# Performance work log

Hardware: AMD Instinct MI355X
Metric: run time of the kernel (lower is better)

The kernel has to match this reference:

```python
import jax, jax.numpy as jnp
import numpy as np

TOPK = 8
N_EXPERTS = 64
ALPHA = 0.001


def setup_inputs() -> dict:
    key = jax.random.key(0)
    k1, k2 = jax.random.split(key)
    B, S, H = 4, 4096, 4096
    x = jax.random.normal(k1, (B, S, H), dtype=jnp.float32)
    # kaiming-uniform-ish router weight, bound = sqrt(6/((1+5)*H)) = 1/sqrt(H)
    bound = 1.0 / np.sqrt(H)
    weight = jax.random.uniform(k2, (N_EXPERTS, H), dtype=jnp.float32,
                                minval=-bound, maxval=bound)
    return {"x": x, "weight": weight}


def reference(x, weight):
    B, S, H = x.shape
    E = weight.shape[0]
    tokens = x.reshape(-1, H)                      # (T, H), T = B*S
    logits = jnp.einsum('th,eh->te', tokens, weight)  # router GEMM (T, E)
    scores = jax.nn.softmax(logits, axis=-1)
    # top-k selection (torch uses sorted=False; same set of values/indices)
    topk_weight, topk_idx = jax.lax.top_k(scores, TOPK)  # (T, k)
    # normalize top-k probs (norm_topk_prob=True, topk>1)
    topk_weight = topk_weight / (topk_weight.sum(axis=1, keepdims=True) + 1e-20)
    # seq-aux load-balancing loss (training path, alpha > 0, seq_aux=True)
    idx_flat = topk_idx.reshape(B, S * TOPK)                 # (B, S*k)
    ce = jax.nn.one_hot(idx_flat, E, dtype=jnp.float32).sum(axis=1)  # scatter_add of ones
    ce = ce / (S * TOPK / E)                                  # (B, E)
    mean_scores = scores.reshape(B, S, E).mean(axis=1)        # (B, E)
    aux_loss = (ce * mean_scores).sum(axis=1).mean() * ALPHA
    return topk_idx, topk_weight, aux_loss
```

## Files before the change

kernel.cpp:

```cpp
#include <hip/hip_runtime.h>
#include <math.h>

#define H 4096
#define NE 64
#define KTOP 8
#define TTOT 16384
#define BT1 32
#define NB1 (TTOT / BT1)
#define BT2 64
#define NB2 (TTOT / BT2)
#define TAU 1e-4f
#define DELTA 1e-3f

typedef __attribute__((ext_vector_type(8))) short bf16x8;
typedef __attribute__((ext_vector_type(4))) float f32x4;

union U4S8 { uint4 u; bf16x8 s; };

__device__ __forceinline__ unsigned bf16_rne(float f) {
  unsigned b = __float_as_uint(f);
  b += 0x7fffu + ((b >> 16) & 1u);
  return b >> 16;
}

__global__ __launch_bounds__(256) void w_prep(const float* __restrict__ w,
                                              uint4* __restrict__ wsimg) {
  const int sid = blockIdx.x * 256 + threadIdx.x;
  const int e = sid >> 9;
  const int rem = sid & 511;
  const int c = rem >> 2;
  const int s = rem & 3;
  const float* src = w + (size_t)e * H + c * 32 + s * 8;
  float4 f0 = *(const float4*)src;
  float4 f1 = *(const float4*)(src + 4);
  float xf[8] = {f0.x, f0.y, f0.z, f0.w, f1.x, f1.y, f1.z, f1.w};
  unsigned hu[8], lu[8];
#pragma unroll
  for (int j = 0; j < 8; ++j) {
    hu[j] = bf16_rne(xf[j]);
    float hf = __uint_as_float(hu[j] << 16);
    lu[j] = bf16_rne(xf[j] - hf);
  }
  uint4 hp, lp;
  hp.x = hu[0] | (hu[1] << 16); hp.y = hu[2] | (hu[3] << 16);
  hp.z = hu[4] | (hu[5] << 16); hp.w = hu[6] | (hu[7] << 16);
  lp.x = lu[0] | (lu[1] << 16); lp.y = lu[2] | (lu[3] << 16);
  lp.z = lu[4] | (lu[5] << 16); lp.w = lu[6] | (lu[7] << 16);
  const int slotp = s ^ ((e >> 1) & 3);
  wsimg[(size_t)c * 256 + e * 4 + slotp] = hp;
  wsimg[(size_t)128 * 256 + (size_t)c * 256 + e * 4 + slotp] = lp;
}

__device__ __forceinline__ void cvt_split(const float4 a, const float4 b,
                                          bf16x8* hi, bf16x8* lo) {
  float xf[8] = {a.x, a.y, a.z, a.w, b.x, b.y, b.z, b.w};
  unsigned ph[4], pl[4];
#pragma unroll
  for (int q = 0; q < 4; ++q)
    asm("v_cvt_pk_bf16_f32 %0, %1, %2" : "=v"(ph[q])
        : "v"(xf[2 * q]), "v"(xf[2 * q + 1]));
  float rs[8];
#pragma unroll
  for (int q = 0; q < 4; ++q) {
    rs[2 * q]     = xf[2 * q]     - __uint_as_float(ph[q] << 16);
    rs[2 * q + 1] = xf[2 * q + 1] - __uint_as_float(ph[q] & 0xffff0000u);
  }
#pragma unroll
  for (int q = 0; q < 4; ++q)
    asm("v_cvt_pk_bf16_f32 %0, %1, %2" : "=v"(pl[q])
        : "v"(rs[2 * q]), "v"(rs[2 * q + 1]));
  U4S8 h, l;
  h.u = (uint4){ph[0], ph[1], ph[2], ph[3]};
  l.u = (uint4){pl[0], pl[1], pl[2], pl[3]};
  *hi = h.s;
  *lo = l.s;
}

#define GLDS(GP, LP)                                                   \
  __builtin_amdgcn_global_load_lds(                                    \
      (const __attribute__((address_space(1))) void*)(GP),             \
      (__attribute__((address_space(3))) void*)(LP), 16, 0, 0)

__global__ __launch_bounds__(128, 1) void moe_pass1(
    const float* __restrict__ x, const uint4* __restrict__ wsimg,
    float* __restrict__ out, unsigned* __restrict__ wmask,
    float* __restrict__ waux) {
  extern __shared__ __align__(16) char smraw[];
  const int tid = threadIdx.x;
  const int lane = tid & 63;
  const int wid = tid >> 6;
  const int tok0 = blockIdx.x * BT1;
  const int trow = lane & 15;
  const int kgrp = lane >> 4;

  const char* xsrc[4];
#pragma unroll
  for (int q = 0; q < 4; ++q) {
    const int a = q * 2048 + tid * 16;
    const int tile = a >> 12;
    const int row = (a >> 8) & 15;
    const int inrow = a & 255;
    const int sin = inrow ^ ((row & 7) << 4);
    xsrc[q] = (const char*)(x + (size_t)(tok0 + tile * 16 + row) * H) + sin;
  }
  const uint4* wsrc[8];
  int wdst[8];
#pragma unroll
  for (int j = 0; j < 8; ++j) {
    const int hilo = j >> 2, sub = (j >> 1) & 1, half = j & 1;
    wsrc[j] = wsimg + (size_t)hilo * (128 * 256) + sub * 256 + half * 128 + tid;
    wdst[j] = 8192 + hilo * 8192 + sub * 4096 + half * 2048 + tid * 16;
  }

  f32x4 acc[4];
#pragma unroll
  for (int et = 0; et < 4; ++et) acc[et] = (f32x4){0.f, 0.f, 0.f, 0.f};

#define ISSUE_STEP(KC, BUF)                                              \
  do {                                                                   \
    char* bb = smraw + (size_t)(BUF) * 24576;                            \
    _Pragma("unroll") for (int q = 0; q < 4; ++q)                        \
      GLDS(xsrc[q] + (size_t)(KC) * 256, bb + q * 2048 + tid * 16);      \
    _Pragma("unroll") for (int j = 0; j < 8; ++j)                        \
      GLDS((const char*)(wsrc[j] + (size_t)(KC) * 512), bb + wdst[j]);   \
  } while (0)

  ISSUE_STEP(0, 0);
  ISSUE_STEP(1, 1);

  const int sx = (trow & 7) << 4;
  const int abase = wid * 4096 + trow * 256;
  int entry[4];
#pragma unroll
  for (int et = 0; et < 4; ++et) {
    const int e = et * 16 + trow;
    entry[et] = (e * 4 + (kgrp ^ ((e >> 1) & 3))) * 16;
  }

#pragma unroll 1
  for (int kc = 0; kc < 64; ++kc) {
    if (kc < 63) {
      asm volatile("s_waitcnt vmcnt(12)" ::: "memory");
    } else {
      asm volatile("s_waitcnt vmcnt(0)" ::: "memory");
    }
    __builtin_amdgcn_s_barrier();
    asm volatile("" ::: "memory");
    if (kc + 2 < 64) ISSUE_STEP(kc + 2, (kc + 2) % 3);

    const char* bufp = smraw + (size_t)(kc % 3) * 24576;
#pragma unroll
    for (int sub = 0; sub < 2; ++sub) {
      float4 v0 = *(const float4*)(bufp + abase + ((sub * 128 + kgrp * 32) ^ sx));
      float4 v1 = *(const float4*)(bufp + abase + ((sub * 128 + kgrp * 32 + 16) ^ sx));
      bf16x8 ah, al;
      cvt_split(v0, v1, &ah, &al);
#pragma unroll
      for (int et = 0; et < 4; ++et) {
        U4S8 bh, bl;
        bh.u = *(const uint4*)(bufp + 8192 + sub * 4096 + entry[et]);
        bl.u = *(const uint4*)(bufp + 16384 + sub * 4096 + entry[et]);
        acc[et] = __builtin_amdgcn_mfma_f32_16x16x32_bf16(ah, bh.s, acc[et], 0, 0, 0);
        acc[et] = __builtin_amdgcn_mfma_f32_16x16x32_bf16(ah, bl.s, acc[et], 0, 0, 0);
        acc[et] = __builtin_amdgcn_mfma_f32_16x16x32_bf16(al, bh.s, acc[et], 0, 0, 0);
      }
    }
  }

  __syncthreads();
  float* lg = (float*)smraw;
  float* msumA = (float*)(smraw + 8448);
  float* cntA = (float*)(smraw + 8960);
#pragma unroll
  for (int et = 0; et < 4; ++et)
#pragma unroll
    for (int r = 0; r < 4; ++r)
      lg[(wid * 16 + kgrp * 4 + r) * 66 + et * 16 + trow] = acc[et][r];
  __syncthreads();

  float msum = 0.f;
  int cnt = 0;
#pragma unroll 1
  for (int it = 0; it < 16; ++it) {
    const int t = wid * 16 + it;
    const float lf = lg[t * 66 + lane];

    float m = lf;
#pragma unroll
    for (int off = 32; off; off >>= 1) m = fmaxf(m, __shfl_xor(m, off));
    float p = expf(lf - m);
    float s = p;
#pragma unroll
    for (int off = 32; off; off >>= 1) s += __shfl_xor(s, off);
    msum += p / s;

    float cur = lf;
    float myv = 0.f;
    int myi = 0;
#pragma unroll
    for (int r = 0; r < 9; ++r) {
      float v = cur;
      int ix = lane;
#pragma unroll
      for (int off = 1; off < 64; off <<= 1) {
        float ov = __shfl_xor(v, off);
        int oi = __shfl_xor(ix, off);
        if (ov > v || (ov == v && oi < ix)) { v = ov; ix = oi; }
      }
      if (lane == r) { myv = v; myi = ix; }
      if (r < 8 && lane == ix) { cur = -INFINITY; ++cnt; }
    }

    const float m0 = __shfl(myv, 0);
    float e = expf(myv - m0);
    float sv = e;
    sv += __shfl_xor(sv, 1);
    sv += __shfl_xor(sv, 2);
    sv += __shfl_xor(sv, 4);
    const float wgtv = e / sv;
    const int tg = tok0 + t;
    if (lane < KTOP) {
      out[(size_t)tg * KTOP + lane] = (float)myi;
      out[(size_t)TTOT * KTOP + (size_t)tg * KTOP + lane] = wgtv;
    }

    const float nxt = __shfl(myv, (lane + 1) & 63);
    const bool gp = (lane < 8) && (myv - nxt < TAU);
    const unsigned long long anyg = __ballot(gp);
    const float v7 = __shfl(myv, 7);
    const unsigned long long msk = __ballot(lf >= v7 - DELTA);
    if (lane == 0) {
      const unsigned long long mv = anyg ? msk : 0ULL;
      wmask[tg] = (unsigned)mv;
      wmask[TTOT + tg] = (unsigned)(mv >> 32);
    }
  }
  msumA[wid * 64 + lane] = msum;
  cntA[wid * 64 + lane] = (float)cnt;
  __syncthreads();
  if (tid < 64) {
    waux[blockIdx.x * 128 + tid] = cntA[tid] + cntA[64 + tid];
    waux[blockIdx.x * 128 + 64 + tid] = msumA[tid] + msumA[64 + tid];
  }
}

__global__ __launch_bounds__(256) void moe_pass2(
    const float* __restrict__ x, const float* __restrict__ w,
    const unsigned* __restrict__ wmask, float* __restrict__ out) {
  __shared__ unsigned slo[64], shi[64];
  __shared__ double red[4];
  __shared__ double cval[64];
  __shared__ int cidx[64];
  const int tid = threadIdx.x;
  const int lane = tid & 63, wid = tid >> 6;
  const int t0 = blockIdx.x * BT2;

  if (tid < 64) { slo[tid] = wmask[t0 + tid]; shi[tid] = wmask[TTOT + t0 + tid]; }
  __syncthreads();
  int myf = (tid < 64) ? ((slo[tid] | shi[tid]) != 0u) : 0;
  if (!__syncthreads_or(myf)) return;

#pragma unroll 1
  for (int tt = 0; tt < BT2; ++tt) {
    const unsigned lo = slo[tt], hi = shi[tt];
    if (!(lo | hi)) continue;
    const int t = t0 + tt;
    const unsigned long long m = ((unsigned long long)hi << 32) | lo;
    const float* xr = x + (size_t)t * H;
    int ncand = 0;
#pragma unroll 1
    for (int e = 0; e < 64; ++e) {
      if (!((m >> e) & 1ULL)) continue;
      const float* wr = w + (size_t)e * H;
      double d = 0.0;
#pragma unroll
      for (int q = 0; q < 16; ++q) {
        const int k = tid + 256 * q;
        d = fma((double)xr[k], (double)wr[k], d);
      }
#pragma unroll
      for (int off = 32; off; off >>= 1) d += __shfl_xor(d, off);
      if (lane == 0) red[wid] = d;
      __syncthreads();
      if (tid == 0) {
        cval[ncand] = red[0] + red[1] + red[2] + red[3];
        cidx[ncand] = e;
      }
      __syncthreads();
      ++ncand;
    }
    if (tid == 0) {
      double sel[8];
      int si[8];
      for (int r = 0; r < 8; ++r) {
        int best = 0;
        double bv = -1e300;
        for (int c2 = 0; c2 < ncand; ++c2)
          if (cval[c2] > bv) { bv = cval[c2]; best = c2; }
        sel[r] = cval[best]; si[r] = cidx[best];
        cval[best] = -1e301;
      }
      const double m0 = sel[0];
      float es[8], ssum = 0.f;
      for (int r = 0; r < 8; ++r) { es[r] = expf((float)(sel[r] - m0)); ssum += es[r]; }
      for (int r = 0; r < 8; ++r) {
        out[(size_t)t * KTOP + r] = (float)si[r];
        out[(size_t)TTOT * KTOP + (size_t)t * KTOP + r] = es[r] / ssum;
      }
    }
    __syncthreads();
  }
}

__global__ __launch_bounds__(256) void moe_gate_aux(
    const float* __restrict__ waux, float* __restrict__ out) {
  const int tid = threadIdx.x;
  const int b = tid >> 6, e = tid & 63;
  float cnt = 0.f, ms = 0.f;
#pragma unroll 4
  for (int j = 0; j < 128; ++j) {
    const int blk = b * 128 + j;
    cnt += waux[blk * 128 + e];
    ms += waux[blk * 128 + 64 + e];
  }
  float term = (cnt * (1.f / 512.f)) * (ms * (1.f / 4096.f));
  __shared__ float red[4];
#pragma unroll
  for (int off = 32; off; off >>= 1) term += __shfl_xor(term, off);
  if ((tid & 63) == 0) red[tid >> 6] = term;
  __syncthreads();
  if (tid == 0) {
    float tot = red[0] + red[1] + red[2] + red[3];
    out[(size_t)TTOT * KTOP * 2] = tot * (0.001f / 4.f);
  }
}

extern "C" void kernel_launch(void* const* d_in, const int* in_sizes, int n_in,
                              void* d_out, int out_size, void* d_ws, size_t ws_size,
                              hipStream_t stream) {
  (void)in_sizes; (void)n_in; (void)out_size; (void)ws_size;
  const float* x = (const float*)d_in[0];
  const float* w = (const float*)d_in[1];
  float* out = (float*)d_out;
  uint4* wsimg = (uint4*)d_ws;
  unsigned* wmask = (unsigned*)((char*)d_ws + (1 << 21));
  float* waux = (float*)((char*)d_ws + (1 << 21) + 2 * TTOT * 4);
  (void)hipFuncSetAttribute((const void*)moe_pass1,
                            hipFuncAttributeMaxDynamicSharedMemorySize, 73728);
  w_prep<<<128, 256, 0, stream>>>(w, wsimg);
  moe_pass1<<<NB1, 128, 73728, stream>>>(x, wsimg, out, wmask, waux);
  moe_pass2<<<NB2, 256, 0, stream>>>(x, w, wmask, out);
  moe_gate_aux<<<1, 256, 0, stream>>>(waux, out);
}
```

Baseline: 246.7 us.

## Restructure router GEMM pass to 1024-thread blocks with per-wave output tiles

The first pass now uses 64-token blocks of 16 waves, with 1024 threads instead of 128. Each wave computes one 16x16 token-by-expert tile. Eight waves stream x and eight stream the pre-split bf16 weight image, each issuing one async global-to-LDS load per 128-byte K step, through a 4-slot ring buffer three steps deep. The goal is more waves in flight to hide HBM latency and less per-thread issue overhead. The cost is twice as many K steps, each with a barrier, a thinner MFMA chain per wave, and a changed aux-reduction layout.

Result: faster. 217.1 us (-12.0%).

```diff
diff --git a/kernel.cpp b/kernel.cpp
--- a/kernel.cpp
+++ b/kernel.cpp
@@ -5,8 +5,9 @@
 #define NE 64
 #define KTOP 8
 #define TTOT 16384
-#define BT1 32
+#define BT1 64
 #define NB1 (TTOT / BT1)
+#define NSTEP 128
 #define BT2 64
 #define NB2 (TTOT / BT2)
 #define TAU 1e-4f
@@ -81,108 +82,93 @@
       (const __attribute__((address_space(1))) void*)(GP),             \
       (__attribute__((address_space(3))) void*)(LP), 16, 0, 0)
 
-__global__ __launch_bounds__(128, 1) void moe_pass1(
+__global__ __launch_bounds__(1024, 1) void moe_pass1(
     const float* __restrict__ x, const uint4* __restrict__ wsimg,
     float* __restrict__ out, unsigned* __restrict__ wmask,
     float* __restrict__ waux) {
   extern __shared__ __align__(16) char smraw[];
   const int tid = threadIdx.x;
   const int lane = tid & 63;
-  const int wid = tid >> 6;
+  const int wv = tid >> 6;
   const int tok0 = blockIdx.x * BT1;
   const int trow = lane & 15;
   const int kgrp = lane >> 4;
 
-  const char* xsrc[4];
-#pragma unroll
-  for (int q = 0; q < 4; ++q) {
-    const int a = q * 2048 + tid * 16;
-    const int tile = a >> 12;
-    const int row = (a >> 8) & 15;
-    const int inrow = a & 255;
+  const char* gsrc;
+  int gadv, ldso;
+  if (wv < 8) {
+    const int row = (wv << 3) + (lane >> 3);
+    const int inrow = (lane & 7) * 16;
     const int sin = inrow ^ ((row & 7) << 4);
-    xsrc[q] = (const char*)(x + (size_t)(tok0 + tile * 16 + row) * H) + sin;
-  }
-  const uint4* wsrc[8];
-  int wdst[8];
-#pragma unroll
-  for (int j = 0; j < 8; ++j) {
-    const int hilo = j >> 2, sub = (j >> 1) & 1, half = j & 1;
-    wsrc[j] = wsimg + (size_t)hilo * (128 * 256) + sub * 256 + half * 128 + tid;
-    wdst[j] = 8192 + hilo * 8192 + sub * 4096 + half * 2048 + tid * 16;
-  }
-
-  f32x4 acc[4];
-#pragma unroll
-  for (int et = 0; et < 4; ++et) acc[et] = (f32x4){0.f, 0.f, 0.f, 0.f};
-
-#define ISSUE_STEP(KC, BUF)                                              \
-  do {                                                                   \
-    char* bb = smraw + (size_t)(BUF) * 24576;                            \
-    _Pragma("unroll") for (int q = 0; q < 4; ++q)                        \
-      GLDS(xsrc[q] + (size_t)(KC) * 256, bb + q * 2048 + tid * 16);      \
-    _Pragma("unroll") for (int j = 0; j < 8; ++j)                        \
-      GLDS((const char*)(wsrc[j] + (size_t)(KC) * 512), bb + wdst[j]);   \
-  } while (0)
-
-  ISSUE_STEP(0, 0);
-  ISSUE_STEP(1, 1);
-
+    gsrc = (const char*)(x + (size_t)(tok0 + row) * H) + sin;
+    gadv = 128;
+    ldso = (wv << 10);
+  } else {
+    const int j = wv - 8;
+    gsrc = (const char*)wsimg + ((j >= 4) ? (512 << 10) : 0) +
+           ((j & 3) << 10) + lane * 16;
+    gadv = 4096;
+    ldso = 8192 + (j << 10);
+  }
+
+#define ISSUE_STEP(KC)                                                  \
+  GLDS(gsrc + (size_t)(KC) * gadv, smraw + (((KC) & 3) << 14) + ldso)
+
+  ISSUE_STEP(0);
+  ISSUE_STEP(1);
+  ISSUE_STEP(2);
+
+  const int tt = wv >> 2;
+  const int et = wv & 3;
+  const int arow = tt * 16 + trow;
   const int sx = (trow & 7) << 4;
-  const int abase = wid * 4096 + trow * 256;
-  int entry[4];
-#pragma unroll
-  for (int et = 0; et < 4; ++et) {
-    const int e = et * 16 + trow;
-    entry[et] = (e * 4 + (kgrp ^ ((e >> 1) & 3))) * 16;
-  }
+  const int abase = arow * 128;
+  const int e = et * 16 + trow;
+  const int eidx = (e * 4 + (kgrp ^ ((e >> 1) & 3))) * 16;
+
+  f32x4 acc = (f32x4){0.f, 0.f, 0.f, 0.f};
 
 #pragma unroll 1
-  for (int kc = 0; kc < 64; ++kc) {
-    if (kc < 63) {
-      asm volatile("s_waitcnt vmcnt(12)" ::: "memory");
+  for (int kc = 0; kc < NSTEP; ++kc) {
+    if (kc <= NSTEP - 3) {
+      asm volatile("s_waitcnt vmcnt(2)" ::: "memory");
+    } else if (kc == NSTEP - 2) {
+      asm volatile("s_waitcnt vmcnt(1)" ::: "memory");
     } else {
       asm volatile("s_waitcnt vmcnt(0)" ::: "memory");
     }
+    asm volatile("s_waitcnt lgkmcnt(0)" ::: "memory");
     __builtin_amdgcn_s_barrier();
     asm volatile("" ::: "memory");
-    if (kc + 2 < 64) ISSUE_STEP(kc + 2, (kc + 2) % 3);
-
-    const char* bufp = smraw + (size_t)(kc % 3) * 24576;
-#pragma unroll
-    for (int sub = 0; sub < 2; ++sub) {
-      float4 v0 = *(const float4*)(bufp + abase + ((sub * 128 + kgrp * 32) ^ sx));
-      float4 v1 = *(const float4*)(bufp + abase + ((sub * 128 + kgrp * 32 + 16) ^ sx));
-      bf16x8 ah, al;
-      cvt_split(v0, v1, &ah, &al);
-#pragma unroll
-      for (int et = 0; et < 4; ++et) {
-        U4S8 bh, bl;
-        bh.u = *(const uint4*)(bufp + 8192 + sub * 4096 + entry[et]);
-        bl.u = *(const uint4*)(bufp + 16384 + sub * 4096 + entry[et]);
-        acc[et] = __builtin_amdgcn_mfma_f32_16x16x32_bf16(ah, bh.s, acc[et], 0, 0, 0);
-        acc[et] = __builtin_amdgcn_mfma_f32_16x16x32_bf16(ah, bl.s, acc[et], 0, 0, 0);
-        acc[et] = __builtin_amdgcn_mfma_f32_16x16x32_bf16(al, bh.s, acc[et], 0, 0, 0);
-      }
-    }
+    if (kc + 3 < NSTEP) ISSUE_STEP(kc + 3);
+
+    const char* slot = smraw + ((kc & 3) << 14);
+    float4 v0 = *(const float4*)(slot + abase + ((kgrp * 32) ^ sx));
+    float4 v1 = *(const float4*)(slot + abase + ((kgrp * 32 + 16) ^ sx));
+    bf16x8 ah, al;
+    cvt_split(v0, v1, &ah, &al);
+    U4S8 bh, bl;
+    bh.u = *(const uint4*)(slot + 8192 + eidx);
+    bl.u = *(const uint4*)(slot + 12288 + eidx);
+    acc = __builtin_amdgcn_mfma_f32_16x16x32_bf16(ah, bh.s, acc, 0, 0, 0);
+    acc = __builtin_amdgcn_mfma_f32_16x16x32_bf16(ah, bl.s, acc, 0, 0, 0);
+    acc = __builtin_amdgcn_mfma_f32_16x16x32_bf16(al, bh.s, acc, 0, 0, 0);
   }
 
   __syncthreads();
   float* lg = (float*)smraw;
-  float* msumA = (float*)(smraw + 8448);
-  float* cntA = (float*)(smraw + 8960);
-#pragma unroll
-  for (int et = 0; et < 4; ++et)
-#pragma unroll
-    for (int r = 0; r < 4; ++r)
-      lg[(wid * 16 + kgrp * 4 + r) * 66 + et * 16 + trow] = acc[et][r];
+  float* msumA = (float*)(smraw + 16896);
+  float* cntA = (float*)(smraw + 20992);
+#pragma unroll
+  for (int r = 0; r < 4; ++r)
+    lg[(tt * 16 + kgrp * 4 + r) * 66 + et * 16 + trow] = acc[r];
   __syncthreads();
 
   float msum = 0.f;
   int cnt = 0;
 #pragma unroll 1
-  for (int it = 0; it < 16; ++it) {
-    const int t = wid * 16 + it;
+  for (int it = 0; it < 4; ++it) {
+    const int t = wv * 4 + it;
     const float lf = lg[t * 66 + lane];
 
     float m = lf;
@@ -212,12 +198,12 @@
     }
 
     const float m0 = __shfl(myv, 0);
-    float e = expf(myv - m0);
-    float sv = e;
+    float ee = expf(myv - m0);
+    float sv = ee;
     sv += __shfl_xor(sv, 1);
     sv += __shfl_xor(sv, 2);
     sv += __shfl_xor(sv, 4);
-    const float wgtv = e / sv;
+    const float wgtv = ee / sv;
     const int tg = tok0 + t;
     if (lane < KTOP) {
       out[(size_t)tg * KTOP + lane] = (float)myi;
@@ -235,12 +221,18 @@
       wmask[TTOT + tg] = (unsigned)(mv >> 32);
     }
   }
-  msumA[wid * 64 + lane] = msum;
-  cntA[wid * 64 + lane] = (float)cnt;
+  msumA[wv * 64 + lane] = msum;
+  cntA[wv * 64 + lane] = (float)cnt;
   __syncthreads();
   if (tid < 64) {
-    waux[blockIdx.x * 128 + tid] = cntA[tid] + cntA[64 + tid];
-    waux[blockIdx.x * 128 + 64 + tid] = msumA[tid] + msumA[64 + tid];
+    float c16 = 0.f, m16 = 0.f;
+#pragma unroll
+    for (int k = 0; k < 16; ++k) {
+      c16 += cntA[k * 64 + tid];
+      m16 += msumA[k * 64 + tid];
+    }
+    waux[blockIdx.x * 128 + tid] = c16;
+    waux[blockIdx.x * 128 + 64 + tid] = m16;
   }
 }
 
@@ -318,8 +310,8 @@
   const int b = tid >> 6, e = tid & 63;
   float cnt = 0.f, ms = 0.f;
 #pragma unroll 4
-  for (int j = 0; j < 128; ++j) {
-    const int blk = b * 128 + j;
+  for (int j = 0; j < 64; ++j) {
+    const int blk = b * 64 + j;
     cnt += waux[blk * 128 + e];
     ms += waux[blk * 128 + 64 + e];
   }
@@ -346,9 +338,9 @@
   unsigned* wmask = (unsigned*)((char*)d_ws + (1 << 21));
   float* waux = (float*)((char*)d_ws + (1 << 21) + 2 * TTOT * 4);
   (void)hipFuncSetAttribute((const void*)moe_pass1,
-                            hipFuncAttributeMaxDynamicSharedMemorySize, 73728);
+                            hipFuncAttributeMaxDynamicSharedMemorySize, 65536);
   w_prep<<<128, 256, 0, stream>>>(w, wsimg);
-  moe_pass1<<<NB1, 128, 73728, stream>>>(x, wsimg, out, wmask, waux);
+  moe_pass1<<<NB1, 1024, 65536, stream>>>(x, wsimg, out, wmask, waux);
   moe_pass2<<<NB2, 256, 0, stream>>>(x, w, wmask, out);
   moe_gate_aux<<<1, 256, 0, stream>>>(waux, out);
 }
```
